# Optimization experiments

Measured on AMD Instinct MI355X. Metric: run time of the kernel, lower is better.

## Reference

```python
import jax, jax.numpy as jnp
import numpy as np

B, N, D, U = 128, 1024, 16, 128


def setup_inputs() -> dict:
    key = jax.random.key(0)
    ks = jax.random.split(key, 12)
    # get_normalized_adj: D^{-1/2} (A + I) D^{-1/2} on a sparse random graph
    A = (jax.random.uniform(ks[0], (N, N)) < 0.01).astype(jnp.float32)
    A = A + jnp.eye(N, dtype=jnp.float32)
    dinv = 1.0 / jnp.sqrt(A.sum(axis=1))
    support = dinv[:, None] * A * dinv[None, :]
    s = 0.05
    return {
        "x": jax.random.normal(ks[1], (2, B, N, D), jnp.float32),
        "hx": jax.random.normal(ks[2], (B, N * U), jnp.float32),
        "delta": jax.random.normal(ks[3], (B, N, D), jnp.float32),
        "support": support,
        "kernel_r": jax.random.normal(ks[4], (D + U, 2 * U), jnp.float32) * jnp.sqrt(2.0 / (D + U)),
        "kernel_c": jax.random.normal(ks[5], (D + U, U), jnp.float32) * jnp.sqrt(2.0 / (D + U)),
        "w_out": jax.random.normal(ks[6], (U + D, D), jnp.float32) * s,
        "b_out": jax.random.normal(ks[7], (D,), jnp.float32) * s,
        "w_basis": jax.random.normal(ks[8], (D, D), jnp.float32) * s,
        "b_basis": jax.random.normal(ks[9], (D,), jnp.float32) * s,
        "lam": jax.random.normal(ks[10], (1,), jnp.float32),
    }


def reference(x, hx, delta, support, kernel_r, kernel_c, w_out, b_out, w_basis, b_basis, lam):
    y_basis, y_res = x[0], x[1]                       # (B, N, D) each
    # speculative delta (add=True branch)
    delta_value = jax.nn.relu(y_res @ w_basis + b_basis)
    p_t = jax.nn.sigmoid(y_res + 0.5 * jnp.sqrt(jnp.abs(delta + 1e-9)))
    new_delta = lam * (2.0 * p_t - 1.0) * delta_value  # (B, N, D)

    hx3 = hx.reshape(B, N, U)

    def gconv(inp, state, kernel):
        # inp (B,N,D), state (B,N,U); diffusion_step == 1 Chebyshev pass
        xs = jnp.concatenate([inp, state], axis=-1)      # (B, N, D+U)
        xs = jnp.einsum('ij,bjl->bil', support, xs)      # diffusion over nodes
        return xs @ kernel                               # (B, N, out)

    value = jax.nn.sigmoid(gconv(y_basis, hx3, kernel_r))  # (B, N, 2U)
    r, u = value[..., :U], value[..., U:]
    c = jnp.tanh(gconv(y_basis, r * hx3, kernel_c))        # (B, N, U)

    u_flat = u.reshape(B, N * U)
    c_flat = c.reshape(B, N * U)
    new_state = hx * u_flat + c_flat * (1.0 - u_flat)      # (B, N*U)

    concat = jnp.concatenate([new_state.reshape(B, N, U), y_basis], axis=-1)
    o = concat @ w_out + b_out + new_delta                 # (B, N, D)
    return (o, new_state, new_delta)
```

## Files before the change

kernel.cpp:

```cpp
#include <hip/hip_runtime.h>
#include <cstdint>

#define B_ 128
#define N_ 1024
#define D_ 16
#define U_ 128
#define M_ (B_*N_)
#define K_ 144
#define KP 192
#define CAP 48

typedef unsigned short u16;
typedef unsigned int   u32;
typedef __attribute__((ext_vector_type(8))) short bf16x8;
typedef __attribute__((ext_vector_type(4))) float f32x4;

__device__ __forceinline__ float bf2f(u16 h){ return __uint_as_float(((u32)h) << 16); }
__device__ __forceinline__ u16 f2bf(float f){
    u32 u = __float_as_uint(f);
    return (u16)((u + 0x7FFFu + ((u >> 16) & 1u)) >> 16);
}
__device__ __forceinline__ float sig_(float x){ return 1.0f / (1.0f + __expf(-x)); }

__global__ void k_ell(const float* __restrict__ sup, float* __restrict__ vals,
                      int* __restrict__ cols, int* __restrict__ nnz,
                      u32* __restrict__ packed)
{
    int wid  = (blockIdx.x * blockDim.x + threadIdx.x) >> 6;
    int lane = threadIdx.x & 63;
    if (wid >= N_) return;
    const float* row = sup + (size_t)wid * N_;
    int base = 0;
    for (int step = 0; step < N_/64; ++step){
        int j = step*64 + lane;
        float v = row[j];
        unsigned long long m = __ballot(v != 0.0f);
        int pos = base + __popcll(m & ((1ull << lane) - 1ull));
        if (v != 0.0f && pos < CAP){
            vals[wid*CAP + pos] = v; cols[wid*CAP + pos] = j;
            if (pos < 16) packed[wid*16 + pos] = ((u32)f2bf(v) << 16) | (u32)j;
        }
        base += __popcll(m);
    }
    int cnt = base < CAP ? base : CAP;
    for (int p = cnt + lane; p < CAP; p += 64){
        vals[wid*CAP + p] = 0.0f;
        cols[wid*CAP + p] = 0;
        if (p < 16) packed[wid*16 + p] = 0;
    }
    if (lane == 0) nnz[wid] = (cnt + 3) & ~3;
}

__global__ void k_prep(const float* __restrict__ kr, const float* __restrict__ kc,
                       u16* __restrict__ wr_t, u16* __restrict__ wc_t)
{
    int t = blockIdx.x * 256 + threadIdx.x;
    if (t < 256*KP){
        int col = t / KP, k = t % KP;
        wr_t[t] = f2bf(k < K_ ? kr[k*256 + col] : 0.0f);
    } else {
        int q = t - 256*KP;
        int col = q / KP, k = q % KP;
        wc_t[q] = f2bf(k < K_ ? kc[k*128 + col] : 0.0f);
    }
}


#define GQB(JJ, WW)                                                            \
    {   uint2 hh = *(const uint2*)(s16 + (int)(JJ)*16 + cq*4);                 \
        float f0 = __uint_as_float(hh.x << 16);                                \
        float f1 = __uint_as_float(hh.x & 0xFFFF0000u);                        \
        float f2 = __uint_as_float(hh.y << 16);                                \
        float f3 = __uint_as_float(hh.y & 0xFFFF0000u);                        \
        acc.x = fmaf((WW), f0, acc.x); acc.y = fmaf((WW), f1, acc.y);          \
        acc.z = fmaf((WW), f2, acc.z); acc.w = fmaf((WW), f3, acc.w); }

#define GQP(EE)                                                                \
    {   u32 e_ = (EE);                                                         \
        float w_ = __uint_as_float(e_ & 0xFFFF0000u);                          \
        GQB(e_ & 1023u, w_) }

#define GB_G(T0)                                                               \
    {   float4 wvt = *(const float4*)(vt + (T0));                              \
        int4   jvt = *(const int4*)(ct + (T0));                                \
        GQB(jvt.x, wvt.x); GQB(jvt.y, wvt.y);                                  \
        GQB(jvt.z, wvt.z); GQB(jvt.w, wvt.w); }

#define GATHER_PACKED(STORE_EXPR)                                              \
    for (int p = tid; p < 4096; p += 512){                                     \
        int node = p >> 2, cq = p & 3;                                         \
        const u32* ep = packed + node*16;                                      \
        uint4 e0 = *(const uint4*)(ep);                                        \
        uint4 e1 = *(const uint4*)(ep + 4);                                    \
        uint4 e2 = *(const uint4*)(ep + 8);                                    \
        uint4 e3 = *(const uint4*)(ep + 12);                                   \
        int c = nnz[node];                                                     \
        float4 acc = make_float4(0.f,0.f,0.f,0.f);                             \
        GQP(e0.x) GQP(e0.y) GQP(e0.z) GQP(e0.w)                                \
        GQP(e1.x) GQP(e1.y) GQP(e1.z) GQP(e1.w)                                \
        GQP(e2.x) GQP(e2.y) GQP(e2.z) GQP(e2.w)                                \
        GQP(e3.x) GQP(e3.y) GQP(e3.z) GQP(e3.w)                                \
        if (c > 16){                                                           \
            const float* vt = vals + node*CAP;                                 \
            const int*   ct = cols + node*CAP;                                 \
            for (int t0 = 16; t0 < c; t0 += 4) GB_G(t0)                        \
        }                                                                      \
        size_t m = (size_t)(b<<10) + node;                                     \
        ushort4 pv; pv.x = f2bf(acc.x); pv.y = f2bf(acc.y);                    \
        pv.z = f2bf(acc.z); pv.w = f2bf(acc.w);                                \
        STORE_EXPR;                                                            \
    }

#define PACK8(PK, VA, VB)                                                      \
    uint4 PK; PK.x = (u32)f2bf((VA).x) | ((u32)f2bf((VA).y) << 16);            \
    PK.y = (u32)f2bf((VA).z) | ((u32)f2bf((VA).w) << 16);                      \
    PK.z = (u32)f2bf((VB).x) | ((u32)f2bf((VB).y) << 16);                      \
    PK.w = (u32)f2bf((VB).z) | ((u32)f2bf((VB).w) << 16);

__global__ __launch_bounds__(512, 8) void k_spmm1(
        const float* __restrict__ x, const float* __restrict__ hx,
        const u32* __restrict__ packed,
        const float* __restrict__ vals, const int* __restrict__ cols,
        const int* __restrict__ nnz, u16* __restrict__ agg)
{
    __shared__ u16 s16[1024*16];
    const int chunk = blockIdx.x;
    const int b     = blockIdx.y;
    const int tid   = threadIdx.x;
    const int cb    = chunk * 16;

    for (int q = tid; q < 2048; q += 512){
        int row = q >> 1, part = q & 1;
        const float* src = (chunk == 0)
            ? &x[((size_t)((b<<10)+row))*16 + part*8]
            : &hx[((size_t)((b<<10)+row))*128 + (cb-16) + part*8];
        float4 va = *(const float4*)src;
        float4 vb = *(const float4*)(src + 4);
        PACK8(pk, va, vb)
        *(uint4*)(s16 + row*16 + part*8) = pk;
    }
    __syncthreads();

    GATHER_PACKED(*(ushort4*)&agg[m*KP + cb + cq*4] = pv)
}

__global__ __launch_bounds__(512, 8) void k_spmm2(
        const u16* __restrict__ value, const float* __restrict__ hx,
        const u32* __restrict__ packed,
        const float* __restrict__ vals, const int* __restrict__ cols,
        const int* __restrict__ nnz, u16* __restrict__ agg)
{
    __shared__ u16 s16[1024*16];
    const int chunk = blockIdx.x;
    const int b     = blockIdx.y;
    const int tid   = threadIdx.x;
    const int cb    = chunk * 16;

    for (int q = tid; q < 2048; q += 512){
        int row = q >> 1, part = q & 1;
        size_t nb = (size_t)((b<<10)+row);
        int hxcol = cb + part*8;
        float4 h0 = *(const float4*)&hx[nb*128 + hxcol];
        float4 h1 = *(const float4*)&hx[nb*128 + hxcol + 4];
        ushort4 r0 = *(const ushort4*)&value[nb*256 + hxcol];
        ushort4 r1 = *(const ushort4*)&value[nb*256 + hxcol + 4];
        float4 va = make_float4(bf2f(r0.x)*h0.x, bf2f(r0.y)*h0.y,
                                bf2f(r0.z)*h0.z, bf2f(r0.w)*h0.w);
        float4 vb = make_float4(bf2f(r1.x)*h1.x, bf2f(r1.y)*h1.y,
                                bf2f(r1.z)*h1.z, bf2f(r1.w)*h1.w);
        PACK8(pk, va, vb)
        *(uint4*)(s16 + row*16 + part*8) = pk;
    }
    __syncthreads();

    GATHER_PACKED(*(ushort4*)&agg[m*KP + D_ + cb + cq*4] = pv)
}

__global__ __launch_bounds__(256) void k_gemm1(const u16* __restrict__ agg,
        const u16* __restrict__ wt, u16* __restrict__ value)
{
    __shared__ u16 a_s[128*168];
    __shared__ u16 w_s[128*72];
    const int rb = blockIdx.x * 128;
    const int tid = threadIdx.x;
    const int wid = tid >> 6, lane = tid & 63;
    const int wr = (wid >> 1) * 64, wc = (wid & 1) * 64;
    const int lrow = lane & 15, lk = (lane >> 4) * 8;
    const int rg = (lane >> 4) * 4;

    for (int q = tid; q < 128*21; q += 256){
        int r_ = q / 21, seg = q % 21;
        uint4 v = {0,0,0,0};
        if (seg < 18) v = *(const uint4*)(agg + (size_t)(rb+r_)*KP + seg*8);
        *(uint4*)(a_s + r_*168 + seg*8) = v;
    }

    for (int half = 0; half < 2; ++half){
        const int cbase = half * 128;
        f32x4 acc[4][4] = {};
        for (int kb = 0; kb < KP; kb += 64){
            __syncthreads();
            #pragma unroll
            for (int i2 = 0; i2 < 4; ++i2){
                int q = tid + i2*256;
                int r_ = q >> 3, sl = q & 7;
                uint4 v = *(const uint4*)(wt + (size_t)(cbase+r_)*KP + kb + sl*8);
                *(uint4*)(w_s + r_*72 + sl*8) = v;
            }
            __syncthreads();
            #pragma unroll
            for (int ks = 0; ks < 2; ++ks){
                bf16x8 af[4], bfv[4];
                #pragma unroll
                for (int f = 0; f < 4; ++f){
                    af[f]  = *(const bf16x8*)(a_s + (wr + f*16 + lrow)*168 + kb + ks*32 + lk);
                    bfv[f] = *(const bf16x8*)(w_s + (wc + f*16 + lrow)*72 + ks*32 + lk);
                }
                #pragma unroll
                for (int fr = 0; fr < 4; ++fr)
                    #pragma unroll
                    for (int fc = 0; fc < 4; ++fc)
                        acc[fr][fc] = __builtin_amdgcn_mfma_f32_16x16x32_bf16(
                            af[fr], bfv[fc], acc[fr][fc], 0, 0, 0);
            }
        }
        #pragma unroll
        for (int fr = 0; fr < 4; ++fr)
            #pragma unroll
            for (int fc = 0; fc < 4; ++fc)
                #pragma unroll
                for (int j = 0; j < 4; ++j){
                    int row = rb + wr + fr*16 + rg + j;
                    int col = cbase + wc + fc*16 + lrow;
                    value[(size_t)row*256 + col] = f2bf(sig_(acc[fr][fc][j]));
                }
    }
}

__global__ __launch_bounds__(256) void k_gemm2(const u16* __restrict__ agg,
        const u16* __restrict__ wt, const float* __restrict__ hx,
        const u16* value, float* ns_out)
{
    __shared__ u16 a_s[128*72];
    __shared__ u16 w_s[128*72];
    const int rb = blockIdx.x * 128;
    const int tid = threadIdx.x;
    const int wid = tid >> 6, lane = tid & 63;
    const int wr = (wid >> 1) * 64, wc = (wid & 1) * 64;
    const int lrow = lane & 15, lk = (lane >> 4) * 8;
    f32x4 acc[4][4] = {};
    for (int kb = 0; kb < KP; kb += 64){
        __syncthreads();
        #pragma unroll
        for (int i2 = 0; i2 < 4; ++i2){
            int q = tid + i2*256;
            int r_ = q >> 3, sl = q & 7;
            uint4 v = {0,0,0,0};
            if (kb + sl*8 < K_)
                v = *(const uint4*)(agg + (size_t)(rb+r_)*KP + kb + sl*8);
            *(uint4*)(a_s + r_*72 + sl*8) = v;
        }
        #pragma unroll
        for (int i2 = 0; i2 < 4; ++i2){
            int q = tid + i2*256;
            int r_ = q >> 3, sl = q & 7;
            uint4 v = *(const uint4*)(wt + (size_t)r_*KP + kb + sl*8);
            *(uint4*)(w_s + r_*72 + sl*8) = v;
        }
        __syncthreads();
        #pragma unroll
        for (int ks = 0; ks < 2; ++ks){
            bf16x8 af[4], bfv[4];
            #pragma unroll
            for (int f = 0; f < 4; ++f){
                af[f]  = *(const bf16x8*)(a_s + (wr + f*16 + lrow)*72 + ks*32 + lk);
                bfv[f] = *(const bf16x8*)(w_s + (wc + f*16 + lrow)*72 + ks*32 + lk);
            }
            #pragma unroll
            for (int fr = 0; fr < 4; ++fr)
                #pragma unroll
                for (int fc = 0; fc < 4; ++fc)
                    acc[fr][fc] = __builtin_amdgcn_mfma_f32_16x16x32_bf16(
                        af[fr], bfv[fc], acc[fr][fc], 0, 0, 0);
        }
    }
    const int rg = (lane >> 4) * 4;
    float ov[4][4][4];
    #pragma unroll
    for (int fr = 0; fr < 4; ++fr)
        #pragma unroll
        for (int fc = 0; fc < 4; ++fc)
            #pragma unroll
            for (int j = 0; j < 4; ++j){
                int row = rb + wr + fr*16 + rg + j;
                int col = wc + fc*16 + lrow;
                float u = bf2f(value[(size_t)row*256 + 128 + col]);
                float h = hx[(size_t)row*128 + col];
                float c = tanhf(acc[fr][fc][j]);
                ov[fr][fc][j] = h*u + c*(1.0f - u);
            }
    __syncthreads();
    #pragma unroll
    for (int fr = 0; fr < 4; ++fr)
        #pragma unroll
        for (int fc = 0; fc < 4; ++fc)
            #pragma unroll
            for (int j = 0; j < 4; ++j){
                int row = rb + wr + fr*16 + rg + j;
                int col = wc + fc*16 + lrow;
                ns_out[(size_t)row*128 + col] = ov[fr][fc][j];
            }
}

__global__ __launch_bounds__(256) void k_out(const float* __restrict__ ns,
        const float* __restrict__ x, const float* __restrict__ delta,
        const float* __restrict__ wo, const float* __restrict__ bo,
        const float* __restrict__ wb, const float* __restrict__ bb,
        const float* __restrict__ lam,
        float* __restrict__ o, float* __restrict__ nd_out)
{
    __shared__ float ns_s[64][132];
    __shared__ float yb_s[64][20];
    __shared__ float yr_s[64][20];
    __shared__ float w_s[144][16];
    __shared__ float wb_s[16][16];
    __shared__ float bo_s[16], bb_s[16];
    int rowbase = blockIdx.x * 64;
    int tid = threadIdx.x;
    const float* yr = x + (size_t)M_ * D_;
    #pragma unroll
    for (int jj = 0; jj < 8; ++jj){
        int q = tid + 256*jj;
        int row = q >> 5, c4 = (q & 31) * 4;
        *(float4*)&ns_s[row][c4] = *(const float4*)&ns[(size_t)(rowbase + row)*U_ + c4];
    }
    {
        int row = tid >> 2, c4 = (tid & 3) * 4;
        *(float4*)&yb_s[row][c4] = *(const float4*)&x[(size_t)(rowbase + row)*D_ + c4];
        *(float4*)&yr_s[row][c4] = *(const float4*)&yr[(size_t)(rowbase + row)*D_ + c4];
    }
    #pragma unroll
    for (int jj = 0; jj < 3; ++jj){
        int q = tid + 256*jj;
        if (q < 576){ int k = q >> 2, d4 = (q & 3) * 4;
            *(float4*)&w_s[k][d4] = *(const float4*)&wo[k*D_ + d4]; }
    }
    wb_s[tid >> 4][tid & 15] = wb[tid];
    if (tid < 16){ bo_s[tid] = bo[tid]; bb_s[tid] = bb[tid]; }
    __syncthreads();
    int row = tid >> 2, d0 = (tid & 3) * 4;
    float4 acc = make_float4(0.f,0.f,0.f,0.f);
    for (int k = 0; k < U_; ++k){
        float cs = ns_s[row][k];
        float4 w = *(const float4*)&w_s[k][d0];
        acc.x = fmaf(cs, w.x, acc.x); acc.y = fmaf(cs, w.y, acc.y);
        acc.z = fmaf(cs, w.z, acc.z); acc.w = fmaf(cs, w.w, acc.w);
    }
    #pragma unroll
    for (int k = 0; k < D_; ++k){
        float cs = yb_s[row][k];
        float4 w = *(const float4*)&w_s[U_ + k][d0];
        acc.x = fmaf(cs, w.x, acc.x); acc.y = fmaf(cs, w.y, acc.y);
        acc.z = fmaf(cs, w.z, acc.z); acc.w = fmaf(cs, w.w, acc.w);
    }
    float4 dacc = make_float4(bb_s[d0], bb_s[d0+1], bb_s[d0+2], bb_s[d0+3]);
    #pragma unroll
    for (int k = 0; k < D_; ++k){
        float yv = yr_s[row][k];
        float4 w = *(const float4*)&wb_s[k][d0];
        dacc.x = fmaf(yv, w.x, dacc.x); dacc.y = fmaf(yv, w.y, dacc.y);
        dacc.z = fmaf(yv, w.z, dacc.z); dacc.w = fmaf(yv, w.w, dacc.w);
    }
    size_t off = (size_t)(rowbase + row)*D_ + d0;
    float4 dl = *(const float4*)&delta[off];
    float lm = lam[0];
    float nd4[4];
    float yv4[4] = {yr_s[row][d0], yr_s[row][d0+1], yr_s[row][d0+2], yr_s[row][d0+3]};
    float dv4[4] = {fmaxf(dacc.x,0.f), fmaxf(dacc.y,0.f), fmaxf(dacc.z,0.f), fmaxf(dacc.w,0.f)};
    float dl4[4] = {dl.x, dl.y, dl.z, dl.w};
    #pragma unroll
    for (int j = 0; j < 4; ++j){
        float pt = sig_(yv4[j] + 0.5f * sqrtf(fabsf(dl4[j] + 1e-9f)));
        nd4[j] = lm * (2.0f * pt - 1.0f) * dv4[j];
    }
    float4 bov = *(const float4*)&bo_s[d0];
    float4 ov = make_float4(acc.x + bov.x + nd4[0], acc.y + bov.y + nd4[1],
                            acc.z + bov.z + nd4[2], acc.w + bov.w + nd4[3]);
    *(float4*)&nd_out[off] = make_float4(nd4[0], nd4[1], nd4[2], nd4[3]);
    *(float4*)&o[off] = ov;
}

extern "C" void kernel_launch(void* const* d_in, const int* in_sizes, int n_in,
                              void* d_out, int out_size, void* d_ws, size_t ws_size,
                              hipStream_t stream)
{
    const float* x        = (const float*)d_in[0];
    const float* hx       = (const float*)d_in[1];
    const float* delta    = (const float*)d_in[2];
    const float* support  = (const float*)d_in[3];
    const float* kernel_r = (const float*)d_in[4];
    const float* kernel_c = (const float*)d_in[5];
    const float* w_out    = (const float*)d_in[6];
    const float* b_out    = (const float*)d_in[7];
    const float* w_basis  = (const float*)d_in[8];
    const float* b_basis  = (const float*)d_in[9];
    const float* lam      = (const float*)d_in[10];

    float* out = (float*)d_out;
    float* o   = out;
    float* ns  = out + 2097152;
    float* nd  = out + 18874368;
    u16*   value = (u16*)ns;

    char* ws = (char*)d_ws;
    float* ell_vals = (float*)ws;
    int*   ell_cols = (int*)(ws + 196608);
    int*   ell_nnz  = (int*)(ws + 393216);
    u32*   ell_pk   = (u32*)(ws + 397312);
    u16*   agg      = (u16*)(ws + (1 << 20));
    u16*   wr_t     = (u16*)(ws + (1 << 20) + (size_t)M_*KP*2);
    u16*   wc_t     = wr_t + 256*KP;

    k_ell  <<<256, 256, 0, stream>>>(support, ell_vals, ell_cols, ell_nnz, ell_pk);
    k_prep <<<(256*KP + 128*KP)/256, 256, 0, stream>>>(kernel_r, kernel_c, wr_t, wc_t);
    k_spmm1<<<dim3(9,128), 512, 0, stream>>>(x, hx, ell_pk,
                                             ell_vals, ell_cols, ell_nnz, agg);
    k_gemm1<<<1024, 256, 0, stream>>>(agg, wr_t, value);
    k_spmm2<<<dim3(8,128), 512, 0, stream>>>(value, hx, ell_pk,
                                             ell_vals, ell_cols, ell_nnz, agg);
    k_gemm2<<<1024, 256, 0, stream>>>(agg, wc_t, hx, value, ns);
    k_out  <<<M_/64, 256, 0, stream>>>(ns, x, delta, w_out, b_out,
                                       w_basis, b_basis, lam, o, nd);
}
```

Measured before the change: 252.8 us.

## Use fp16 dot2 gathers in SpMM, split gemm1 columns across blocks, merge prep kernels

The SpMM staging buffers now hold fp16 instead of bf16, and the packed ELL entries carry fp16 weights. Pairs of neighbours are combined with packed dot2 instructions, which roughly halves the FMA and unpack work in the gather. gemm1 now streams A through a smaller shared tile and splits the 256 output columns over a second grid dimension, which cuts LDS use and raises block count at the cost of loading A twice. The ELL build and weight-transpose prep are merged into one launch. fp16 has less range than bf16 in the aggregated values, and the SpMM outputs are still written as bf16.

```diff
diff --git a/kernel.cpp b/kernel.cpp
--- a/kernel.cpp
+++ b/kernel.cpp
@@ -14,18 +14,57 @@
 typedef unsigned int   u32;
 typedef __attribute__((ext_vector_type(8))) short bf16x8;
 typedef __attribute__((ext_vector_type(4))) float f32x4;
+typedef __attribute__((ext_vector_type(2))) __fp16 h2v;
 
 __device__ __forceinline__ float bf2f(u16 h){ return __uint_as_float(((u32)h) << 16); }
 __device__ __forceinline__ u16 f2bf(float f){
     u32 u = __float_as_uint(f);
     return (u16)((u + 0x7FFFu + ((u >> 16) & 1u)) >> 16);
 }
+__device__ __forceinline__ u16 f2h(float f){
+    __fp16 h = (__fp16)f; u16 s; __builtin_memcpy(&s, &h, 2); return s;
+}
+__device__ __forceinline__ float h2f_lo(u32 u){
+    u16 s = (u16)(u & 0xFFFFu); __fp16 h; __builtin_memcpy(&h, &s, 2); return (float)h;
+}
+__device__ __forceinline__ float h2f_hi(u32 u){
+    u16 s = (u16)(u >> 16); __fp16 h; __builtin_memcpy(&h, &s, 2); return (float)h;
+}
+__device__ __forceinline__ u32 pkrtz(float a, float b){
+    h2v r = __builtin_amdgcn_cvt_pkrtz(a, b);
+    u32 v; __builtin_memcpy(&v, &r, 4); return v;
+}
 __device__ __forceinline__ float sig_(float x){ return 1.0f / (1.0f + __expf(-x)); }
 
-__global__ void k_ell(const float* __restrict__ sup, float* __restrict__ vals,
-                      int* __restrict__ cols, int* __restrict__ nnz,
-                      u32* __restrict__ packed)
-{
+#if __has_builtin(__builtin_amdgcn_fdot2)
+__device__ __forceinline__ float dot2_(u32 a, u32 b, float c){
+    h2v av, bv; __builtin_memcpy(&av, &a, 4); __builtin_memcpy(&bv, &b, 4);
+    return __builtin_amdgcn_fdot2(av, bv, c, false);
+}
+#else
+__device__ __forceinline__ float dot2_(u32 a, u32 b, float c){
+    return fmaf(h2f_hi(a), h2f_hi(b), fmaf(h2f_lo(a), h2f_lo(b), c));
+}
+#endif
+
+__global__ void k_ellprep(const float* __restrict__ sup,
+                          const float* __restrict__ kr, const float* __restrict__ kc,
+                          float* __restrict__ vals, int* __restrict__ cols,
+                          int* __restrict__ nnz, u32* __restrict__ packed,
+                          u16* __restrict__ wr_t, u16* __restrict__ wc_t)
+{
+    if (blockIdx.x >= 256){
+        int t = (blockIdx.x - 256) * 256 + threadIdx.x;
+        if (t < 256*KP){
+            int col = t / KP, k = t % KP;
+            wr_t[t] = f2bf(k < K_ ? kr[k*256 + col] : 0.0f);
+        } else {
+            int q = t - 256*KP;
+            int col = q / KP, k = q % KP;
+            wc_t[q] = f2bf(k < K_ ? kc[k*128 + col] : 0.0f);
+        }
+        return;
+    }
     int wid  = (blockIdx.x * blockDim.x + threadIdx.x) >> 6;
     int lane = threadIdx.x & 63;
     if (wid >= N_) return;
@@ -38,7 +77,7 @@
         int pos = base + __popcll(m & ((1ull << lane) - 1ull));
         if (v != 0.0f && pos < CAP){
             vals[wid*CAP + pos] = v; cols[wid*CAP + pos] = j;
-            if (pos < 16) packed[wid*16 + pos] = ((u32)f2bf(v) << 16) | (u32)j;
+            if (pos < 16) packed[wid*16 + pos] = (u32)f2h(v) | ((u32)j << 16);
         }
         base += __popcll(m);
     }
@@ -51,40 +90,31 @@
     if (lane == 0) nnz[wid] = (cnt + 3) & ~3;
 }
 
-__global__ void k_prep(const float* __restrict__ kr, const float* __restrict__ kc,
-                       u16* __restrict__ wr_t, u16* __restrict__ wc_t)
-{
-    int t = blockIdx.x * 256 + threadIdx.x;
-    if (t < 256*KP){
-        int col = t / KP, k = t % KP;
-        wr_t[t] = f2bf(k < K_ ? kr[k*256 + col] : 0.0f);
-    } else {
-        int q = t - 256*KP;
-        int col = q / KP, k = q % KP;
-        wc_t[q] = f2bf(k < K_ ? kc[k*128 + col] : 0.0f);
-    }
-}
-
-
-#define GQB(JJ, WW)                                                            \
+
+#define GQD(E0, E1)                                                            \
+    {   u32 wp = __builtin_amdgcn_perm((E1), (E0), 0x05040100u);               \
+        int c0 = (int)((E0) >> 16), c1 = (int)((E1) >> 16);                    \
+        uint2 hh0 = *(const uint2*)(s16 + c0*16 + cq*4);                       \
+        uint2 hh1 = *(const uint2*)(s16 + c1*16 + cq*4);                       \
+        u32 pa0 = __builtin_amdgcn_perm(hh1.x, hh0.x, 0x05040100u);            \
+        u32 pa1 = __builtin_amdgcn_perm(hh1.x, hh0.x, 0x07060302u);            \
+        u32 pa2 = __builtin_amdgcn_perm(hh1.y, hh0.y, 0x05040100u);            \
+        u32 pa3 = __builtin_amdgcn_perm(hh1.y, hh0.y, 0x07060302u);            \
+        acc.x = dot2_(wp, pa0, acc.x); acc.y = dot2_(wp, pa1, acc.y);          \
+        acc.z = dot2_(wp, pa2, acc.z); acc.w = dot2_(wp, pa3, acc.w); }
+
+#define GQH(JJ, WW)                                                            \
     {   uint2 hh = *(const uint2*)(s16 + (int)(JJ)*16 + cq*4);                 \
-        float f0 = __uint_as_float(hh.x << 16);                                \
-        float f1 = __uint_as_float(hh.x & 0xFFFF0000u);                        \
-        float f2 = __uint_as_float(hh.y << 16);                                \
-        float f3 = __uint_as_float(hh.y & 0xFFFF0000u);                        \
-        acc.x = fmaf((WW), f0, acc.x); acc.y = fmaf((WW), f1, acc.y);          \
-        acc.z = fmaf((WW), f2, acc.z); acc.w = fmaf((WW), f3, acc.w); }
-
-#define GQP(EE)                                                                \
-    {   u32 e_ = (EE);                                                         \
-        float w_ = __uint_as_float(e_ & 0xFFFF0000u);                          \
-        GQB(e_ & 1023u, w_) }
+        acc.x = fmaf((WW), h2f_lo(hh.x), acc.x);                               \
+        acc.y = fmaf((WW), h2f_hi(hh.x), acc.y);                               \
+        acc.z = fmaf((WW), h2f_lo(hh.y), acc.z);                               \
+        acc.w = fmaf((WW), h2f_hi(hh.y), acc.w); }
 
 #define GB_G(T0)                                                               \
     {   float4 wvt = *(const float4*)(vt + (T0));                              \
         int4   jvt = *(const int4*)(ct + (T0));                                \
-        GQB(jvt.x, wvt.x); GQB(jvt.y, wvt.y);                                  \
-        GQB(jvt.z, wvt.z); GQB(jvt.w, wvt.w); }
+        GQH(jvt.x, wvt.x); GQH(jvt.y, wvt.y);                                  \
+        GQH(jvt.z, wvt.z); GQH(jvt.w, wvt.w); }
 
 #define GATHER_PACKED(STORE_EXPR)                                              \
     for (int p = tid; p < 4096; p += 512){                                     \
@@ -96,10 +126,10 @@
         uint4 e3 = *(const uint4*)(ep + 12);                                   \
         int c = nnz[node];                                                     \
         float4 acc = make_float4(0.f,0.f,0.f,0.f);                             \
-        GQP(e0.x) GQP(e0.y) GQP(e0.z) GQP(e0.w)                                \
-        GQP(e1.x) GQP(e1.y) GQP(e1.z) GQP(e1.w)                                \
-        GQP(e2.x) GQP(e2.y) GQP(e2.z) GQP(e2.w)                                \
-        GQP(e3.x) GQP(e3.y) GQP(e3.z) GQP(e3.w)                                \
+        GQD(e0.x, e0.y) GQD(e0.z, e0.w)                                        \
+        GQD(e1.x, e1.y) GQD(e1.z, e1.w)                                        \
+        GQD(e2.x, e2.y) GQD(e2.z, e2.w)                                        \
+        GQD(e3.x, e3.y) GQD(e3.z, e3.w)                                        \
         if (c > 16){                                                           \
             const float* vt = vals + node*CAP;                                 \
             const int*   ct = cols + node*CAP;                                 \
@@ -111,11 +141,9 @@
         STORE_EXPR;                                                            \
     }
 
-#define PACK8(PK, VA, VB)                                                      \
-    uint4 PK; PK.x = (u32)f2bf((VA).x) | ((u32)f2bf((VA).y) << 16);            \
-    PK.y = (u32)f2bf((VA).z) | ((u32)f2bf((VA).w) << 16);                      \
-    PK.z = (u32)f2bf((VB).x) | ((u32)f2bf((VB).y) << 16);                      \
-    PK.w = (u32)f2bf((VB).z) | ((u32)f2bf((VB).w) << 16);
+#define PACKH8(PK, VA, VB)                                                     \
+    uint4 PK; PK.x = pkrtz((VA).x, (VA).y); PK.y = pkrtz((VA).z, (VA).w);      \
+    PK.z = pkrtz((VB).x, (VB).y); PK.w = pkrtz((VB).z, (VB).w);
 
 __global__ __launch_bounds__(512, 8) void k_spmm1(
         const float* __restrict__ x, const float* __restrict__ hx,
@@ -136,7 +164,7 @@
             : &hx[((size_t)((b<<10)+row))*128 + (cb-16) + part*8];
         float4 va = *(const float4*)src;
         float4 vb = *(const float4*)(src + 4);
-        PACK8(pk, va, vb)
+        PACKH8(pk, va, vb)
         *(uint4*)(s16 + row*16 + part*8) = pk;
     }
     __syncthreads();
@@ -168,7 +196,7 @@
                                 bf2f(r0.z)*h0.z, bf2f(r0.w)*h0.w);
         float4 vb = make_float4(bf2f(r1.x)*h1.x, bf2f(r1.y)*h1.y,
                                 bf2f(r1.z)*h1.z, bf2f(r1.w)*h1.w);
-        PACK8(pk, va, vb)
+        PACKH8(pk, va, vb)
         *(uint4*)(s16 + row*16 + part*8) = pk;
     }
     __syncthreads();
@@ -179,62 +207,60 @@
 __global__ __launch_bounds__(256) void k_gemm1(const u16* __restrict__ agg,
         const u16* __restrict__ wt, u16* __restrict__ value)
 {
-    __shared__ u16 a_s[128*168];
+    __shared__ u16 a_s[128*72];
     __shared__ u16 w_s[128*72];
-    const int rb = blockIdx.x * 128;
+    const int rb = blockIdx.x * 128, cb = blockIdx.y * 128;
     const int tid = threadIdx.x;
     const int wid = tid >> 6, lane = tid & 63;
     const int wr = (wid >> 1) * 64, wc = (wid & 1) * 64;
     const int lrow = lane & 15, lk = (lane >> 4) * 8;
+    f32x4 acc[4][4] = {};
+    for (int kb = 0; kb < KP; kb += 64){
+        __syncthreads();
+        #pragma unroll
+        for (int i2 = 0; i2 < 4; ++i2){
+            int q = tid + i2*256;
+            int r_ = q >> 3, sl = q & 7;
+            uint4 v = {0,0,0,0};
+            if (kb + sl*8 < K_)
+                v = *(const uint4*)(agg + (size_t)(rb+r_)*KP + kb + sl*8);
+            *(uint4*)(a_s + r_*72 + sl*8) = v;
+        }
+        #pragma unroll
+        for (int i2 = 0; i2 < 4; ++i2){
+            int q = tid + i2*256;
+            int r_ = q >> 3, sl = q & 7;
+            uint4 v = *(const uint4*)(wt + (size_t)(cb+r_)*KP + kb + sl*8);
+            *(uint4*)(w_s + r_*72 + sl*8) = v;
+        }
+        __syncthreads();
+        #pragma unroll
+        for (int ks = 0; ks < 2; ++ks){
+            bf16x8 af[4], bfv[4];
+            #pragma unroll
+            for (int f = 0; f < 4; ++f){
+                af[f]  = *(const bf16x8*)(a_s + (wr + f*16 + lrow)*72 + ks*32 + lk);
+                bfv[f] = *(const bf16x8*)(w_s + (wc + f*16 + lrow)*72 + ks*32 + lk);
+            }
+            #pragma unroll
+            for (int fr = 0; fr < 4; ++fr)
+                #pragma unroll
+                for (int fc = 0; fc < 4; ++fc)
+                    acc[fr][fc] = __builtin_amdgcn_mfma_f32_16x16x32_bf16(
+                        af[fr], bfv[fc], acc[fr][fc], 0, 0, 0);
+        }
+    }
     const int rg = (lane >> 4) * 4;
-
-    for (int q = tid; q < 128*21; q += 256){
-        int r_ = q / 21, seg = q % 21;
-        uint4 v = {0,0,0,0};
-        if (seg < 18) v = *(const uint4*)(agg + (size_t)(rb+r_)*KP + seg*8);
-        *(uint4*)(a_s + r_*168 + seg*8) = v;
-    }
-
-    for (int half = 0; half < 2; ++half){
-        const int cbase = half * 128;
-        f32x4 acc[4][4] = {};
-        for (int kb = 0; kb < KP; kb += 64){
-            __syncthreads();
-            #pragma unroll
-            for (int i2 = 0; i2 < 4; ++i2){
-                int q = tid + i2*256;
-                int r_ = q >> 3, sl = q & 7;
-                uint4 v = *(const uint4*)(wt + (size_t)(cbase+r_)*KP + kb + sl*8);
-                *(uint4*)(w_s + r_*72 + sl*8) = v;
+    #pragma unroll
+    for (int fr = 0; fr < 4; ++fr)
+        #pragma unroll
+        for (int fc = 0; fc < 4; ++fc)
+            #pragma unroll
+            for (int j = 0; j < 4; ++j){
+                int row = rb + wr + fr*16 + rg + j;
+                int col = cb + wc + fc*16 + lrow;
+                value[(size_t)row*256 + col] = f2bf(sig_(acc[fr][fc][j]));
             }
-            __syncthreads();
-            #pragma unroll
-            for (int ks = 0; ks < 2; ++ks){
-                bf16x8 af[4], bfv[4];
-                #pragma unroll
-                for (int f = 0; f < 4; ++f){
-                    af[f]  = *(const bf16x8*)(a_s + (wr + f*16 + lrow)*168 + kb + ks*32 + lk);
-                    bfv[f] = *(const bf16x8*)(w_s + (wc + f*16 + lrow)*72 + ks*32 + lk);
-                }
-                #pragma unroll
-                for (int fr = 0; fr < 4; ++fr)
-                    #pragma unroll
-                    for (int fc = 0; fc < 4; ++fc)
-                        acc[fr][fc] = __builtin_amdgcn_mfma_f32_16x16x32_bf16(
-                            af[fr], bfv[fc], acc[fr][fc], 0, 0, 0);
-            }
-        }
-        #pragma unroll
-        for (int fr = 0; fr < 4; ++fr)
-            #pragma unroll
-            for (int fc = 0; fc < 4; ++fc)
-                #pragma unroll
-                for (int j = 0; j < 4; ++j){
-                    int row = rb + wr + fr*16 + rg + j;
-                    int col = cbase + wc + fc*16 + lrow;
-                    value[(size_t)row*256 + col] = f2bf(sig_(acc[fr][fc][j]));
-                }
-    }
 }
 
 __global__ __launch_bounds__(256) void k_gemm2(const u16* __restrict__ agg,
@@ -421,14 +447,15 @@
     u16*   wr_t     = (u16*)(ws + (1 << 20) + (size_t)M_*KP*2);
     u16*   wc_t     = wr_t + 256*KP;
 
-    k_ell  <<<256, 256, 0, stream>>>(support, ell_vals, ell_cols, ell_nnz, ell_pk);
-    k_prep <<<(256*KP + 128*KP)/256, 256, 0, stream>>>(kernel_r, kernel_c, wr_t, wc_t);
+    k_ellprep<<<544, 256, 0, stream>>>(support, kernel_r, kernel_c,
+                                       ell_vals, ell_cols, ell_nnz, ell_pk,
+                                       wr_t, wc_t);
     k_spmm1<<<dim3(9,128), 512, 0, stream>>>(x, hx, ell_pk,
                                              ell_vals, ell_cols, ell_nnz, agg);
-    k_gemm1<<<1024, 256, 0, stream>>>(agg, wr_t, value);
+    k_gemm1<<<dim3(M_/128, 2), 256, 0, stream>>>(agg, wr_t, value);
     k_spmm2<<<dim3(8,128), 512, 0, stream>>>(value, hx, ell_pk,
                                              ell_vals, ell_cols, ell_nnz, agg);
-    k_gemm2<<<1024, 256, 0, stream>>>(agg, wc_t, hx, value, ns);
+    k_gemm2<<<M_/128, 256, 0, stream>>>(agg, wc_t, hx, value, ns);
     k_out  <<<M_/64, 256, 0, stream>>>(ns, x, delta, w_out, b_out,
                                        w_basis, b_basis, lam, o, nd);
 }
```

After: 228.7 us. -9.5%, faster.
